# Kernel optimization log

Measured on AMD Instinct MI355X. Metric: run time of the kernel, lower is better.

Reference implementation:

```python
import jax, jax.numpy as jnp
import numpy as np

B = 65536
LAYERS = [256, 512, 512, 256]


def setup_inputs() -> dict:
    key = jax.random.key(0)
    ks = jax.random.split(key, 10)
    inp = {"data": jax.random.normal(ks[0], (B, LAYERS[0]), dtype=jnp.float32)}
    for i in range(3):
        n_in, n_out = LAYERS[i], LAYERS[i + 1]
        # link weights ~ U[0,1) like random.random(); bias params[0] zeroed in torch code
        inp[f"W{i+1}"] = jax.random.uniform(ks[1 + 3 * i], (n_in, n_out), dtype=jnp.float32)
        inp[f"b{i+1}"] = jnp.zeros((n_out,), dtype=jnp.float32)
        # per-node activation params a = params[1:6], torch.rand init
        inp[f"a{i+1}"] = jax.random.uniform(ks[2 + 3 * i], (n_out, 5), dtype=jnp.float32)
    return inp


def _act(x, a):
    # x: [B, n], a: [n, 5]; a0*tanh(x)*sin(a1*x+a2) + a3*x + a4  (per-node params broadcast over batch)
    return a[:, 0] * jnp.tanh(x) * jnp.sin(a[:, 1] * x + a[:, 2]) + a[:, 3] * x + a[:, 4]


def reference(data, W1, b1, a1, W2, b2, a2, W3, b3, a3):
    h = _act(data @ W1 + b1, a1)
    h = _act(h @ W2 + b2, a2)
    h = _act(h @ W3 + b3, a3)
    return jax.nn.softmax(h, axis=1)
```

## Files before the change

### kernel.cpp

```cpp
#include <hip/hip_runtime.h>

#define BATCH 65536

typedef float f32x4 __attribute__((ext_vector_type(4)));
typedef _Float16 f16x8 __attribute__((ext_vector_type(8)));

__device__ __forceinline__ void async_ld16(const void* g, void* l) {
  __builtin_amdgcn_global_load_lds(
      (const __attribute__((address_space(1))) void*)g,
      (__attribute__((address_space(3))) void*)l, 16, 0, 0);
}

__device__ __forceinline__ float act_f(float x, float a0, float a1, float a2,
                                       float a3, float a4) {
  float ax = fabsf(x);
  float e = __builtin_amdgcn_exp2f(ax * -2.8853900817779268f);
  float th = (1.0f - e) * __builtin_amdgcn_rcpf(1.0f + e);
  th = copysignf(th, x);
  float arg = fmaf(a1, x, a2);
  float rev = arg * 0.15915494309189535f;
  rev -= floorf(rev);
  float s = __builtin_amdgcn_sinf(rev);
  return fmaf(a3, x, fmaf(a0 * th, s, a4));
}

__global__ __launch_bounds__(256) void splitT_k(const float* __restrict__ W,
                                                _Float16* __restrict__ hi,
                                                _Float16* __restrict__ lo,
                                                int K, int N) {
  const int i = blockIdx.x * 256 + threadIdx.x;
  if (i >= K * N) return;
  const int n = i / K, k = i % K;
  const float w = W[(size_t)k * N + n];
  const _Float16 h = (_Float16)w;
  hi[i] = h;
  lo[i] = (_Float16)(w - (float)h);
}

__device__ __forceinline__ f32x4 mfma3(f16x8 ah, f16x8 al, f16x8 bh, f16x8 bl,
                                       f32x4 c) {
  c = __builtin_amdgcn_mfma_f32_16x16x32_f16(ah, bh, c, 0, 0, 0);
  c = __builtin_amdgcn_mfma_f32_16x16x32_f16(ah, bl, c, 0, 0, 0);
  c = __builtin_amdgcn_mfma_f32_16x16x32_f16(al, bh, c, 0, 0, 0);
  return c;
}

template <bool AF32, bool FINAL>
__global__ __launch_bounds__(256, 4) void gemm_act(
    const float* __restrict__ Af, const _Float16* __restrict__ Ahi,
    const _Float16* __restrict__ Alo, const _Float16* __restrict__ Bhi,
    const _Float16* __restrict__ Blo, const float* __restrict__ bias,
    const float* __restrict__ ap, _Float16* __restrict__ Chi,
    _Float16* __restrict__ Clo, float* __restrict__ Cout, int K, int N) {
  __shared__ __align__(16) _Float16 sA[4096];
  __shared__ __align__(16) _Float16 sB[16384];

  const int tid = threadIdx.x;
  const int wv = tid >> 6;
  const int lane = tid & 63;
  const int wm = wv >> 1, wn = wv & 1;
  const int m16 = lane & 15, quad = lane >> 4;
  const int col0 = blockIdx.x * 256;
  const int row0 = blockIdx.y * 64;

  f32x4 acc[2][8];
  const f32x4 zero = {0.f, 0.f, 0.f, 0.f};
#pragma unroll
  for (int i = 0; i < 2; ++i)
#pragma unroll
    for (int j = 0; j < 8; ++j) acc[i][j] = zero;

  const int nk = K >> 5;
  for (int kt = 0; kt < nk; ++kt) {
    const int k0 = kt << 5;
    if (AF32) {
      float* sAf = (float*)sA;
#pragma unroll
      for (int t = 0; t < 2; ++t) {
        const int c = wv * 2 + t;
        const int r = c * 8 + (lane >> 3);
        const size_t ga = (size_t)(row0 + r) * K + k0 + (lane & 7) * 4;
        async_ld16(Af + ga, (void*)&sAf[c * 256]);
      }
    } else {
      const int r = wv * 16 + (lane >> 2);
      const size_t ga = (size_t)(row0 + r) * K + k0 + (lane & 3) * 8;
      async_ld16(Ahi + ga, (void*)&sA[wv * 512]);
      async_ld16(Alo + ga, (void*)&sA[2048 + wv * 512]);
    }
#pragma unroll
    for (int t = 0; t < 4; ++t) {
      const int c = wv * 4 + t;
      const int col = c * 16 + (lane >> 2);
      const size_t gb = (size_t)(col0 + col) * K + k0 + (lane & 3) * 8;
      async_ld16(Bhi + gb, (void*)&sB[c * 512]);
      async_ld16(Blo + gb, (void*)&sB[8192 + c * 512]);
    }
    __syncthreads();

    f16x8 ah[2], al[2];
#pragma unroll
    for (int tm = 0; tm < 2; ++tm) {
      const int arow = wm * 32 + tm * 16 + m16;
      if (AF32) {
        const float* pa = (const float*)sA + arow * 32 + quad * 8;
        const f32x4 x0 = *(const f32x4*)pa;
        const f32x4 x1 = *(const f32x4*)(pa + 4);
#pragma unroll
        for (int j = 0; j < 4; ++j) {
          const _Float16 h0 = (_Float16)x0[j];
          ah[tm][j] = h0;
          al[tm][j] = (_Float16)(x0[j] - (float)h0);
          const _Float16 h1 = (_Float16)x1[j];
          ah[tm][4 + j] = h1;
          al[tm][4 + j] = (_Float16)(x1[j] - (float)h1);
        }
      } else {
        ah[tm] = *(const f16x8*)&sA[arow * 32 + quad * 8];
        al[tm] = *(const f16x8*)&sA[2048 + arow * 32 + quad * 8];
      }
    }
#pragma unroll
    for (int tn = 0; tn < 8; ++tn) {
      const int bcol = wn * 128 + tn * 16 + m16;
      const f16x8 bh = *(const f16x8*)&sB[bcol * 32 + quad * 8];
      const f16x8 bl = *(const f16x8*)&sB[8192 + bcol * 32 + quad * 8];
#pragma unroll
      for (int tm = 0; tm < 2; ++tm)
        acc[tm][tn] = mfma3(ah[tm], al[tm], bh, bl, acc[tm][tn]);
    }
    __syncthreads();
  }

  if (FINAL) {
    float* const redf = (float*)sA;
    float* const rowm = (float*)sA + 128;
    float* const rowi = (float*)sA + 192;
#pragma unroll
    for (int tn = 0; tn < 8; ++tn) {
      const int col = col0 + wn * 128 + tn * 16 + m16;
      const float bs = bias[col];
      const float p0 = ap[col * 5 + 0];
      const float p1 = ap[col * 5 + 1];
      const float p2 = ap[col * 5 + 2];
      const float p3 = ap[col * 5 + 3];
      const float p4 = ap[col * 5 + 4];
#pragma unroll
      for (int tm = 0; tm < 2; ++tm)
#pragma unroll
        for (int r = 0; r < 4; ++r)
          acc[tm][tn][r] = act_f(acc[tm][tn][r] + bs, p0, p1, p2, p3, p4);
    }
#pragma unroll
    for (int tm = 0; tm < 2; ++tm)
#pragma unroll
      for (int r = 0; r < 4; ++r) {
        float m = acc[tm][0][r];
#pragma unroll
        for (int tn = 1; tn < 8; ++tn) m = fmaxf(m, acc[tm][tn][r]);
#pragma unroll
        for (int off = 1; off < 16; off <<= 1) m = fmaxf(m, __shfl_xor(m, off));
        if (m16 == 0) {
          const int rowl = wm * 32 + tm * 16 + quad * 4 + r;
          redf[wn * 64 + rowl] = m;
        }
      }
    __syncthreads();
    if (tid < 64) rowm[tid] = fmaxf(redf[tid], redf[64 + tid]);
    __syncthreads();
#pragma unroll
    for (int tm = 0; tm < 2; ++tm)
#pragma unroll
      for (int r = 0; r < 4; ++r) {
        const int rowl = wm * 32 + tm * 16 + quad * 4 + r;
        const float m = rowm[rowl];
        float s = 0.f;
#pragma unroll
        for (int tn = 0; tn < 8; ++tn) {
          const float e = __builtin_amdgcn_exp2f((acc[tm][tn][r] - m) *
                                                 1.4426950408889634f);
          acc[tm][tn][r] = e;
          s += e;
        }
#pragma unroll
        for (int off = 1; off < 16; off <<= 1) s += __shfl_xor(s, off);
        if (m16 == 0) redf[wn * 64 + rowl] = s;
      }
    __syncthreads();
    if (tid < 64) rowi[tid] = __builtin_amdgcn_rcpf(redf[tid] + redf[64 + tid]);
    __syncthreads();
#pragma unroll
    for (int tm = 0; tm < 2; ++tm)
#pragma unroll
      for (int r = 0; r < 4; ++r) {
        const int rowl = wm * 32 + tm * 16 + quad * 4 + r;
        const float inv = rowi[rowl];
#pragma unroll
        for (int tn = 0; tn < 8; ++tn) {
          const int col = col0 + wn * 128 + tn * 16 + m16;
          Cout[(size_t)(row0 + rowl) * 256 + col] = acc[tm][tn][r] * inv;
        }
      }
  } else {
#pragma unroll
    for (int tn = 0; tn < 8; ++tn) {
      const int col = col0 + wn * 128 + tn * 16 + m16;
      const float bs = bias[col];
      const float p0 = ap[col * 5 + 0];
      const float p1 = ap[col * 5 + 1];
      const float p2 = ap[col * 5 + 2];
      const float p3 = ap[col * 5 + 3];
      const float p4 = ap[col * 5 + 4];
#pragma unroll
      for (int tm = 0; tm < 2; ++tm) {
        const int row = row0 + wm * 32 + tm * 16 + quad * 4;
#pragma unroll
        for (int r = 0; r < 4; ++r) {
          const float y = act_f(acc[tm][tn][r] + bs, p0, p1, p2, p3, p4);
          const size_t o = (size_t)(row + r) * N + col;
          const _Float16 h = (_Float16)y;
          Chi[o] = h;
          Clo[o] = (_Float16)(y - (float)h);
        }
      }
    }
  }
}

extern "C" void kernel_launch(void* const* d_in, const int* in_sizes, int n_in,
                              void* d_out, int out_size, void* d_ws,
                              size_t ws_size, hipStream_t stream) {
  const float* data = (const float*)d_in[0];
  const float* W1 = (const float*)d_in[1];
  const float* b1 = (const float*)d_in[2];
  const float* a1 = (const float*)d_in[3];
  const float* W2 = (const float*)d_in[4];
  const float* b2 = (const float*)d_in[5];
  const float* a2 = (const float*)d_in[6];
  const float* W3 = (const float*)d_in[7];
  const float* b3 = (const float*)d_in[8];
  const float* a3 = (const float*)d_in[9];
  float* out = (float*)d_out;

  char* ws = (char*)d_ws;
  const size_t KB = 1024, MB = 1024 * 1024;
  _Float16* w1hi = (_Float16*)(ws + 0 * KB);
  _Float16* w1lo = (_Float16*)(ws + 256 * KB);
  _Float16* w2hi = (_Float16*)(ws + 512 * KB);
  _Float16* w2lo = (_Float16*)(ws + 1024 * KB);
  _Float16* w3hi = (_Float16*)(ws + 1536 * KB);
  _Float16* w3lo = (_Float16*)(ws + 1792 * KB);
  _Float16* h1hi = (_Float16*)(ws + 2 * MB);
  _Float16* h1lo = (_Float16*)(ws + 2 * MB + (size_t)BATCH * 512 * 2);
  _Float16* h2lo = (_Float16*)(ws + 2 * MB + (size_t)BATCH * 512 * 4);
  _Float16* h2hi = (_Float16*)d_out;

  splitT_k<<<(256 * 512 + 255) / 256, 256, 0, stream>>>(W1, w1hi, w1lo, 256, 512);
  splitT_k<<<(512 * 512 + 255) / 256, 256, 0, stream>>>(W2, w2hi, w2lo, 512, 512);
  splitT_k<<<(512 * 256 + 255) / 256, 256, 0, stream>>>(W3, w3hi, w3lo, 512, 256);

  gemm_act<true, false><<<dim3(2, BATCH / 64), 256, 0, stream>>>(
      data, nullptr, nullptr, w1hi, w1lo, b1, a1, h1hi, h1lo, nullptr, 256, 512);
  gemm_act<false, false><<<dim3(2, BATCH / 64), 256, 0, stream>>>(
      nullptr, h1hi, h1lo, w2hi, w2lo, b2, a2, h2hi, h2lo, nullptr, 512, 512);
  gemm_act<false, true><<<dim3(1, BATCH / 64), 256, 0, stream>>>(
      nullptr, h2hi, h2lo, w3hi, w3lo, b3, a3, nullptr, nullptr, out, 512, 256);
}
```

Baseline: 427.2 us.

## Use square 128x128 tiles with XOR-swizzled LDS for hidden layers

Splits the templated kernel into a 128x128-tile kernel for the first two layers and a dedicated 64x256 kernel for the final layer with softmax. The square tiles are meant to balance A and B reuse and reduce global traffic per MFMA, and an XOR swizzle on the LDS chunk index is meant to remove bank conflicts on the fragment reads. The trade-offs are more accumulator registers per wave (16 tiles) and twice the A staging space at the same occupancy target.

```diff
diff --git a/kernel.cpp b/kernel.cpp
--- a/kernel.cpp
+++ b/kernel.cpp
@@ -45,30 +45,31 @@
   return c;
 }
 
-template <bool AF32, bool FINAL>
-__global__ __launch_bounds__(256, 4) void gemm_act(
+template <bool AF32>
+__global__ __launch_bounds__(256, 4) void gemm128(
     const float* __restrict__ Af, const _Float16* __restrict__ Ahi,
     const _Float16* __restrict__ Alo, const _Float16* __restrict__ Bhi,
     const _Float16* __restrict__ Blo, const float* __restrict__ bias,
     const float* __restrict__ ap, _Float16* __restrict__ Chi,
-    _Float16* __restrict__ Clo, float* __restrict__ Cout, int K, int N) {
-  __shared__ __align__(16) _Float16 sA[4096];
-  __shared__ __align__(16) _Float16 sB[16384];
+    _Float16* __restrict__ Clo, int K, int N) {
+  __shared__ __align__(16) _Float16 sA[8192];
+  __shared__ __align__(16) _Float16 sB[8192];
 
   const int tid = threadIdx.x;
   const int wv = tid >> 6;
   const int lane = tid & 63;
   const int wm = wv >> 1, wn = wv & 1;
   const int m16 = lane & 15, quad = lane >> 4;
-  const int col0 = blockIdx.x * 256;
-  const int row0 = blockIdx.y * 64;
-
-  f32x4 acc[2][8];
+  const int qsw = quad ^ (m16 & 3);
+  const int col0 = blockIdx.x * 128;
+  const int row0 = blockIdx.y * 128;
+
+  f32x4 acc[4][4];
   const f32x4 zero = {0.f, 0.f, 0.f, 0.f};
 #pragma unroll
-  for (int i = 0; i < 2; ++i)
-#pragma unroll
-    for (int j = 0; j < 8; ++j) acc[i][j] = zero;
+  for (int i = 0; i < 4; ++i)
+#pragma unroll
+    for (int j = 0; j < 4; ++j) acc[i][j] = zero;
 
   const int nk = K >> 5;
   for (int kt = 0; kt < nk; ++kt) {
@@ -76,36 +77,45 @@
     if (AF32) {
       float* sAf = (float*)sA;
 #pragma unroll
+      for (int t = 0; t < 4; ++t) {
+        const int c = wv * 4 + t;
+        const int r = c * 8 + (lane >> 3);
+        const int sl = (lane & 7) ^ (r & 7);
+        const size_t ga = (size_t)(row0 + r) * K + k0 + sl * 4;
+        async_ld16(Af + ga, (void*)&sAf[c * 256]);
+      }
+    } else {
+#pragma unroll
       for (int t = 0; t < 2; ++t) {
         const int c = wv * 2 + t;
-        const int r = c * 8 + (lane >> 3);
-        const size_t ga = (size_t)(row0 + r) * K + k0 + (lane & 7) * 4;
-        async_ld16(Af + ga, (void*)&sAf[c * 256]);
-      }
-    } else {
-      const int r = wv * 16 + (lane >> 2);
-      const size_t ga = (size_t)(row0 + r) * K + k0 + (lane & 3) * 8;
-      async_ld16(Ahi + ga, (void*)&sA[wv * 512]);
-      async_ld16(Alo + ga, (void*)&sA[2048 + wv * 512]);
-    }
-#pragma unroll
-    for (int t = 0; t < 4; ++t) {
-      const int c = wv * 4 + t;
+        const int r = c * 16 + (lane >> 2);
+        const int sl = (lane & 3) ^ (r & 3);
+        const size_t ga = (size_t)(row0 + r) * K + k0 + sl * 8;
+        async_ld16(Ahi + ga, (void*)&sA[c * 512]);
+        async_ld16(Alo + ga, (void*)&sA[4096 + c * 512]);
+      }
+    }
+#pragma unroll
+    for (int t = 0; t < 2; ++t) {
+      const int c = wv * 2 + t;
       const int col = c * 16 + (lane >> 2);
-      const size_t gb = (size_t)(col0 + col) * K + k0 + (lane & 3) * 8;
+      const int sl = (lane & 3) ^ (col & 3);
+      const size_t gb = (size_t)(col0 + col) * K + k0 + sl * 8;
       async_ld16(Bhi + gb, (void*)&sB[c * 512]);
-      async_ld16(Blo + gb, (void*)&sB[8192 + c * 512]);
+      async_ld16(Blo + gb, (void*)&sB[4096 + c * 512]);
     }
     __syncthreads();
 
-    f16x8 ah[2], al[2];
-#pragma unroll
-    for (int tm = 0; tm < 2; ++tm) {
-      const int arow = wm * 32 + tm * 16 + m16;
+    f16x8 ah[4], al[4];
+#pragma unroll
+    for (int tm = 0; tm < 4; ++tm) {
+      const int arow = wm * 64 + tm * 16 + m16;
       if (AF32) {
-        const float* pa = (const float*)sA + arow * 32 + quad * 8;
-        const f32x4 x0 = *(const f32x4*)pa;
-        const f32x4 x1 = *(const f32x4*)(pa + 4);
+        const float* pa = (const float*)sA + arow * 32;
+        const int s0 = (2 * quad) ^ (m16 & 7);
+        const int s1 = (2 * quad + 1) ^ (m16 & 7);
+        const f32x4 x0 = *(const f32x4*)(pa + s0 * 4);
+        const f32x4 x1 = *(const f32x4*)(pa + s1 * 4);
 #pragma unroll
         for (int j = 0; j < 4; ++j) {
           const _Float16 h0 = (_Float16)x0[j];
@@ -116,9 +126,93 @@
           al[tm][4 + j] = (_Float16)(x1[j] - (float)h1);
         }
       } else {
-        ah[tm] = *(const f16x8*)&sA[arow * 32 + quad * 8];
-        al[tm] = *(const f16x8*)&sA[2048 + arow * 32 + quad * 8];
-      }
+        ah[tm] = *(const f16x8*)&sA[arow * 32 + qsw * 8];
+        al[tm] = *(const f16x8*)&sA[4096 + arow * 32 + qsw * 8];
+      }
+    }
+#pragma unroll
+    for (int tn = 0; tn < 4; ++tn) {
+      const int bcol = wn * 64 + tn * 16 + m16;
+      const f16x8 bh = *(const f16x8*)&sB[bcol * 32 + qsw * 8];
+      const f16x8 bl = *(const f16x8*)&sB[4096 + bcol * 32 + qsw * 8];
+#pragma unroll
+      for (int tm = 0; tm < 4; ++tm)
+        acc[tm][tn] = mfma3(ah[tm], al[tm], bh, bl, acc[tm][tn]);
+    }
+    __syncthreads();
+  }
+
+#pragma unroll
+  for (int tn = 0; tn < 4; ++tn) {
+    const int col = col0 + wn * 64 + tn * 16 + m16;
+    const float bs = bias[col];
+    const float p0 = ap[col * 5 + 0];
+    const float p1 = ap[col * 5 + 1];
+    const float p2 = ap[col * 5 + 2];
+    const float p3 = ap[col * 5 + 3];
+    const float p4 = ap[col * 5 + 4];
+#pragma unroll
+    for (int tm = 0; tm < 4; ++tm) {
+      const int row = row0 + wm * 64 + tm * 16 + quad * 4;
+#pragma unroll
+      for (int r = 0; r < 4; ++r) {
+        const float y = act_f(acc[tm][tn][r] + bs, p0, p1, p2, p3, p4);
+        const size_t o = (size_t)(row + r) * N + col;
+        const _Float16 h = (_Float16)y;
+        Chi[o] = h;
+        Clo[o] = (_Float16)(y - (float)h);
+      }
+    }
+  }
+}
+
+__global__ __launch_bounds__(256, 4) void gemm_final(
+    const _Float16* __restrict__ Ahi, const _Float16* __restrict__ Alo,
+    const _Float16* __restrict__ Bhi, const _Float16* __restrict__ Blo,
+    const float* __restrict__ bias, const float* __restrict__ ap,
+    float* __restrict__ Cout, int K) {
+  __shared__ __align__(16) _Float16 sA[4096];
+  __shared__ __align__(16) _Float16 sB[16384];
+
+  const int tid = threadIdx.x;
+  const int wv = tid >> 6;
+  const int lane = tid & 63;
+  const int wm = wv >> 1, wn = wv & 1;
+  const int m16 = lane & 15, quad = lane >> 4;
+  const int row0 = blockIdx.x * 64;
+
+  f32x4 acc[2][8];
+  const f32x4 zero = {0.f, 0.f, 0.f, 0.f};
+#pragma unroll
+  for (int i = 0; i < 2; ++i)
+#pragma unroll
+    for (int j = 0; j < 8; ++j) acc[i][j] = zero;
+
+  const int nk = K >> 5;
+  for (int kt = 0; kt < nk; ++kt) {
+    const int k0 = kt << 5;
+    {
+      const int r = wv * 16 + (lane >> 2);
+      const size_t ga = (size_t)(row0 + r) * K + k0 + (lane & 3) * 8;
+      async_ld16(Ahi + ga, (void*)&sA[wv * 512]);
+      async_ld16(Alo + ga, (void*)&sA[2048 + wv * 512]);
+    }
+#pragma unroll
+    for (int t = 0; t < 4; ++t) {
+      const int c = wv * 4 + t;
+      const int col = c * 16 + (lane >> 2);
+      const size_t gb = (size_t)col * K + k0 + (lane & 3) * 8;
+      async_ld16(Bhi + gb, (void*)&sB[c * 512]);
+      async_ld16(Blo + gb, (void*)&sB[8192 + c * 512]);
+    }
+    __syncthreads();
+
+    f16x8 ah[2], al[2];
+#pragma unroll
+    for (int tm = 0; tm < 2; ++tm) {
+      const int arow = wm * 32 + tm * 16 + m16;
+      ah[tm] = *(const f16x8*)&sA[arow * 32 + quad * 8];
+      al[tm] = *(const f16x8*)&sA[2048 + arow * 32 + quad * 8];
     }
 #pragma unroll
     for (int tn = 0; tn < 8; ++tn) {
@@ -132,99 +226,74 @@
     __syncthreads();
   }
 
-  if (FINAL) {
-    float* const redf = (float*)sA;
-    float* const rowm = (float*)sA + 128;
-    float* const rowi = (float*)sA + 192;
-#pragma unroll
-    for (int tn = 0; tn < 8; ++tn) {
-      const int col = col0 + wn * 128 + tn * 16 + m16;
-      const float bs = bias[col];
-      const float p0 = ap[col * 5 + 0];
-      const float p1 = ap[col * 5 + 1];
-      const float p2 = ap[col * 5 + 2];
-      const float p3 = ap[col * 5 + 3];
-      const float p4 = ap[col * 5 + 4];
-#pragma unroll
-      for (int tm = 0; tm < 2; ++tm)
-#pragma unroll
-        for (int r = 0; r < 4; ++r)
-          acc[tm][tn][r] = act_f(acc[tm][tn][r] + bs, p0, p1, p2, p3, p4);
-    }
+  float* const redf = (float*)sA;
+  float* const rowm = (float*)sA + 128;
+  float* const rowi = (float*)sA + 192;
+#pragma unroll
+  for (int tn = 0; tn < 8; ++tn) {
+    const int col = wn * 128 + tn * 16 + m16;
+    const float bs = bias[col];
+    const float p0 = ap[col * 5 + 0];
+    const float p1 = ap[col * 5 + 1];
+    const float p2 = ap[col * 5 + 2];
+    const float p3 = ap[col * 5 + 3];
+    const float p4 = ap[col * 5 + 4];
 #pragma unroll
     for (int tm = 0; tm < 2; ++tm)
 #pragma unroll
-      for (int r = 0; r < 4; ++r) {
-        float m = acc[tm][0][r];
-#pragma unroll
-        for (int tn = 1; tn < 8; ++tn) m = fmaxf(m, acc[tm][tn][r]);
-#pragma unroll
-        for (int off = 1; off < 16; off <<= 1) m = fmaxf(m, __shfl_xor(m, off));
-        if (m16 == 0) {
-          const int rowl = wm * 32 + tm * 16 + quad * 4 + r;
-          redf[wn * 64 + rowl] = m;
-        }
-      }
-    __syncthreads();
-    if (tid < 64) rowm[tid] = fmaxf(redf[tid], redf[64 + tid]);
-    __syncthreads();
-#pragma unroll
-    for (int tm = 0; tm < 2; ++tm)
-#pragma unroll
-      for (int r = 0; r < 4; ++r) {
+      for (int r = 0; r < 4; ++r)
+        acc[tm][tn][r] = act_f(acc[tm][tn][r] + bs, p0, p1, p2, p3, p4);
+  }
+#pragma unroll
+  for (int tm = 0; tm < 2; ++tm)
+#pragma unroll
+    for (int r = 0; r < 4; ++r) {
+      float m = acc[tm][0][r];
+#pragma unroll
+      for (int tn = 1; tn < 8; ++tn) m = fmaxf(m, acc[tm][tn][r]);
+#pragma unroll
+      for (int off = 1; off < 16; off <<= 1) m = fmaxf(m, __shfl_xor(m, off));
+      if (m16 == 0) {
         const int rowl = wm * 32 + tm * 16 + quad * 4 + r;
-        const float m = rowm[rowl];
-        float s = 0.f;
-#pragma unroll
-        for (int tn = 0; tn < 8; ++tn) {
-          const float e = __builtin_amdgcn_exp2f((acc[tm][tn][r] - m) *
-                                                 1.4426950408889634f);
-          acc[tm][tn][r] = e;
-          s += e;
-        }
-#pragma unroll
-        for (int off = 1; off < 16; off <<= 1) s += __shfl_xor(s, off);
-        if (m16 == 0) redf[wn * 64 + rowl] = s;
-      }
-    __syncthreads();
-    if (tid < 64) rowi[tid] = __builtin_amdgcn_rcpf(redf[tid] + redf[64 + tid]);
-    __syncthreads();
-#pragma unroll
-    for (int tm = 0; tm < 2; ++tm)
-#pragma unroll
-      for (int r = 0; r < 4; ++r) {
-        const int rowl = wm * 32 + tm * 16 + quad * 4 + r;
-        const float inv = rowi[rowl];
-#pragma unroll
-        for (int tn = 0; tn < 8; ++tn) {
-          const int col = col0 + wn * 128 + tn * 16 + m16;
-          Cout[(size_t)(row0 + rowl) * 256 + col] = acc[tm][tn][r] * inv;
-        }
-      }
-  } else {
-#pragma unroll
-    for (int tn = 0; tn < 8; ++tn) {
-      const int col = col0 + wn * 128 + tn * 16 + m16;
-      const float bs = bias[col];
-      const float p0 = ap[col * 5 + 0];
-      const float p1 = ap[col * 5 + 1];
-      const float p2 = ap[col * 5 + 2];
-      const float p3 = ap[col * 5 + 3];
-      const float p4 = ap[col * 5 + 4];
-#pragma unroll
-      for (int tm = 0; tm < 2; ++tm) {
-        const int row = row0 + wm * 32 + tm * 16 + quad * 4;
-#pragma unroll
-        for (int r = 0; r < 4; ++r) {
-          const float y = act_f(acc[tm][tn][r] + bs, p0, p1, p2, p3, p4);
-          const size_t o = (size_t)(row + r) * N + col;
-          const _Float16 h = (_Float16)y;
-          Chi[o] = h;
-          Clo[o] = (_Float16)(y - (float)h);
-        }
-      }
-    }
-  }
+        redf[wn * 64 + rowl] = m;
+      }
+    }
+  __syncthreads();
+  if (tid < 64) rowm[tid] = fmaxf(redf[tid], redf[64 + tid]);
+  __syncthreads();
+#pragma unroll
+  for (int tm = 0; tm < 2; ++tm)
+#pragma unroll
+    for (int r = 0; r < 4; ++r) {
+      const int rowl = wm * 32 + tm * 16 + quad * 4 + r;
+      const float m = rowm[rowl];
+      float s = 0.f;
+#pragma unroll
+      for (int tn = 0; tn < 8; ++tn) {
+        const float e =
+            __builtin_amdgcn_exp2f((acc[tm][tn][r] - m) * 1.4426950408889634f);
+        acc[tm][tn][r] = e;
+        s += e;
+      }
+#pragma unroll
+      for (int off = 1; off < 16; off <<= 1) s += __shfl_xor(s, off);
+      if (m16 == 0) redf[wn * 64 + rowl] = s;
+    }
+  __syncthreads();
+  if (tid < 64) rowi[tid] = __builtin_amdgcn_rcpf(redf[tid] + redf[64 + tid]);
+  __syncthreads();
+#pragma unroll
+  for (int tm = 0; tm < 2; ++tm)
+#pragma unroll
+    for (int r = 0; r < 4; ++r) {
+      const int rowl = wm * 32 + tm * 16 + quad * 4 + r;
+      const float inv = rowi[rowl];
+#pragma unroll
+      for (int tn = 0; tn < 8; ++tn) {
+        const int col = wn * 128 + tn * 16 + m16;
+        Cout[(size_t)(row0 + rowl) * 256 + col] = acc[tm][tn][r] * inv;
+      }
+    }
 }
 
 extern "C" void kernel_launch(void* const* d_in, const int* in_sizes, int n_in,
@@ -259,10 +328,10 @@
   splitT_k<<<(512 * 512 + 255) / 256, 256, 0, stream>>>(W2, w2hi, w2lo, 512, 512);
   splitT_k<<<(512 * 256 + 255) / 256, 256, 0, stream>>>(W3, w3hi, w3lo, 512, 256);
 
-  gemm_act<true, false><<<dim3(2, BATCH / 64), 256, 0, stream>>>(
-      data, nullptr, nullptr, w1hi, w1lo, b1, a1, h1hi, h1lo, nullptr, 256, 512);
-  gemm_act<false, false><<<dim3(2, BATCH / 64), 256, 0, stream>>>(
-      nullptr, h1hi, h1lo, w2hi, w2lo, b2, a2, h2hi, h2lo, nullptr, 512, 512);
-  gemm_act<false, true><<<dim3(1, BATCH / 64), 256, 0, stream>>>(
-      nullptr, h2hi, h2lo, w3hi, w3lo, b3, a3, nullptr, nullptr, out, 512, 256);
-}
+  gemm128<true><<<dim3(4, BATCH / 128), 256, 0, stream>>>(
+      data, nullptr, nullptr, w1hi, w1lo, b1, a1, h1hi, h1lo, 256, 512);
+  gemm128<false><<<dim3(4, BATCH / 128), 256, 0, stream>>>(
+      nullptr, h1hi, h1lo, w2hi, w2lo, b2, a2, h2hi, h2lo, 512, 512);
+  gemm_final<<<BATCH / 64, 256, 0, stream>>>(h2hi, h2lo, w3hi, w3lo, b3, a3,
+                                             out, 512);
+}
```

Measured after the change: 496.5 us. +16.2%, slower.

## Enlarge GEMM block tile to 128x256 with 8 waves and XOR-swizzle LDS

Applied to the files above, without the earlier changes.

Doubles the block tile to 128 rows by 256 columns using 512 threads (2x4 waves, each computing a 64x64 sub-tile), so weight tiles are reused across twice as many rows. It also XOR-swizzles the 16-byte chunk positions in LDS for both A and B, on the async store side and the read side, to reduce bank conflicts on the MFMA operand loads. The softmax reduction is widened to combine four column-wave partials. The cost is more LDS per block and launch bounds of 512x4, which may push register pressure and lower occupancy.

```diff
diff --git a/kernel.cpp b/kernel.cpp
--- a/kernel.cpp
+++ b/kernel.cpp
@@ -46,29 +46,30 @@
 }
 
 template <bool AF32, bool FINAL>
-__global__ __launch_bounds__(256, 4) void gemm_act(
+__global__ __launch_bounds__(512, 4) void gemm_act(
     const float* __restrict__ Af, const _Float16* __restrict__ Ahi,
     const _Float16* __restrict__ Alo, const _Float16* __restrict__ Bhi,
     const _Float16* __restrict__ Blo, const float* __restrict__ bias,
     const float* __restrict__ ap, _Float16* __restrict__ Chi,
     _Float16* __restrict__ Clo, float* __restrict__ Cout, int K, int N) {
-  __shared__ __align__(16) _Float16 sA[4096];
+  __shared__ __align__(16) _Float16 sA[8192];
   __shared__ __align__(16) _Float16 sB[16384];
 
   const int tid = threadIdx.x;
   const int wv = tid >> 6;
   const int lane = tid & 63;
-  const int wm = wv >> 1, wn = wv & 1;
+  const int wm = wv >> 2, wn = wv & 3;
   const int m16 = lane & 15, quad = lane >> 4;
+  const int qsw = quad ^ (m16 & 3);
   const int col0 = blockIdx.x * 256;
-  const int row0 = blockIdx.y * 64;
-
-  f32x4 acc[2][8];
+  const int row0 = blockIdx.y * 128;
+
+  f32x4 acc[4][4];
   const f32x4 zero = {0.f, 0.f, 0.f, 0.f};
 #pragma unroll
-  for (int i = 0; i < 2; ++i)
-#pragma unroll
-    for (int j = 0; j < 8; ++j) acc[i][j] = zero;
+  for (int i = 0; i < 4; ++i)
+#pragma unroll
+    for (int j = 0; j < 4; ++j) acc[i][j] = zero;
 
   const int nk = K >> 5;
   for (int kt = 0; kt < nk; ++kt) {
@@ -79,33 +80,38 @@
       for (int t = 0; t < 2; ++t) {
         const int c = wv * 2 + t;
         const int r = c * 8 + (lane >> 3);
-        const size_t ga = (size_t)(row0 + r) * K + k0 + (lane & 7) * 4;
+        const int sl = (lane & 7) ^ (r & 7);
+        const size_t ga = (size_t)(row0 + r) * K + k0 + sl * 4;
         async_ld16(Af + ga, (void*)&sAf[c * 256]);
       }
     } else {
       const int r = wv * 16 + (lane >> 2);
-      const size_t ga = (size_t)(row0 + r) * K + k0 + (lane & 3) * 8;
+      const int sl = (lane & 3) ^ (r & 3);
+      const size_t ga = (size_t)(row0 + r) * K + k0 + sl * 8;
       async_ld16(Ahi + ga, (void*)&sA[wv * 512]);
-      async_ld16(Alo + ga, (void*)&sA[2048 + wv * 512]);
-    }
-#pragma unroll
-    for (int t = 0; t < 4; ++t) {
-      const int c = wv * 4 + t;
+      async_ld16(Alo + ga, (void*)&sA[4096 + wv * 512]);
+    }
+#pragma unroll
+    for (int t = 0; t < 2; ++t) {
+      const int c = wv * 2 + t;
       const int col = c * 16 + (lane >> 2);
-      const size_t gb = (size_t)(col0 + col) * K + k0 + (lane & 3) * 8;
+      const int sl = (lane & 3) ^ (col & 3);
+      const size_t gb = (size_t)(col0 + col) * K + k0 + sl * 8;
       async_ld16(Bhi + gb, (void*)&sB[c * 512]);
       async_ld16(Blo + gb, (void*)&sB[8192 + c * 512]);
     }
     __syncthreads();
 
-    f16x8 ah[2], al[2];
-#pragma unroll
-    for (int tm = 0; tm < 2; ++tm) {
-      const int arow = wm * 32 + tm * 16 + m16;
+    f16x8 ah[4], al[4];
+#pragma unroll
+    for (int tm = 0; tm < 4; ++tm) {
+      const int arow = wm * 64 + tm * 16 + m16;
       if (AF32) {
-        const float* pa = (const float*)sA + arow * 32 + quad * 8;
-        const f32x4 x0 = *(const f32x4*)pa;
-        const f32x4 x1 = *(const f32x4*)(pa + 4);
+        const float* pa = (const float*)sA + arow * 32;
+        const int s0 = (2 * quad) ^ (m16 & 7);
+        const int s1 = (2 * quad + 1) ^ (m16 & 7);
+        const f32x4 x0 = *(const f32x4*)(pa + s0 * 4);
+        const f32x4 x1 = *(const f32x4*)(pa + s1 * 4);
 #pragma unroll
         for (int j = 0; j < 4; ++j) {
           const _Float16 h0 = (_Float16)x0[j];
@@ -116,17 +122,17 @@
           al[tm][4 + j] = (_Float16)(x1[j] - (float)h1);
         }
       } else {
-        ah[tm] = *(const f16x8*)&sA[arow * 32 + quad * 8];
-        al[tm] = *(const f16x8*)&sA[2048 + arow * 32 + quad * 8];
-      }
-    }
-#pragma unroll
-    for (int tn = 0; tn < 8; ++tn) {
-      const int bcol = wn * 128 + tn * 16 + m16;
-      const f16x8 bh = *(const f16x8*)&sB[bcol * 32 + quad * 8];
-      const f16x8 bl = *(const f16x8*)&sB[8192 + bcol * 32 + quad * 8];
-#pragma unroll
-      for (int tm = 0; tm < 2; ++tm)
+        ah[tm] = *(const f16x8*)&sA[arow * 32 + qsw * 8];
+        al[tm] = *(const f16x8*)&sA[4096 + arow * 32 + qsw * 8];
+      }
+    }
+#pragma unroll
+    for (int tn = 0; tn < 4; ++tn) {
+      const int bcol = wn * 64 + tn * 16 + m16;
+      const f16x8 bh = *(const f16x8*)&sB[bcol * 32 + qsw * 8];
+      const f16x8 bl = *(const f16x8*)&sB[8192 + bcol * 32 + qsw * 8];
+#pragma unroll
+      for (int tm = 0; tm < 4; ++tm)
         acc[tm][tn] = mfma3(ah[tm], al[tm], bh, bl, acc[tm][tn]);
     }
     __syncthreads();
@@ -134,11 +140,11 @@
 
   if (FINAL) {
     float* const redf = (float*)sA;
-    float* const rowm = (float*)sA + 128;
-    float* const rowi = (float*)sA + 192;
-#pragma unroll
-    for (int tn = 0; tn < 8; ++tn) {
-      const int col = col0 + wn * 128 + tn * 16 + m16;
+    float* const rowm = (float*)sA + 512;
+    float* const rowi = (float*)sA + 640;
+#pragma unroll
+    for (int tn = 0; tn < 4; ++tn) {
+      const int col = wn * 64 + tn * 16 + m16;
       const float bs = bias[col];
       const float p0 = ap[col * 5 + 0];
       const float p1 = ap[col * 5 + 1];
@@ -146,37 +152,38 @@
       const float p3 = ap[col * 5 + 3];
       const float p4 = ap[col * 5 + 4];
 #pragma unroll
-      for (int tm = 0; tm < 2; ++tm)
+      for (int tm = 0; tm < 4; ++tm)
 #pragma unroll
         for (int r = 0; r < 4; ++r)
           acc[tm][tn][r] = act_f(acc[tm][tn][r] + bs, p0, p1, p2, p3, p4);
     }
 #pragma unroll
-    for (int tm = 0; tm < 2; ++tm)
+    for (int tm = 0; tm < 4; ++tm)
 #pragma unroll
       for (int r = 0; r < 4; ++r) {
-        float m = acc[tm][0][r];
-#pragma unroll
-        for (int tn = 1; tn < 8; ++tn) m = fmaxf(m, acc[tm][tn][r]);
+        float m = fmaxf(fmaxf(acc[tm][0][r], acc[tm][1][r]),
+                        fmaxf(acc[tm][2][r], acc[tm][3][r]));
 #pragma unroll
         for (int off = 1; off < 16; off <<= 1) m = fmaxf(m, __shfl_xor(m, off));
         if (m16 == 0) {
-          const int rowl = wm * 32 + tm * 16 + quad * 4 + r;
-          redf[wn * 64 + rowl] = m;
-        }
-      }
-    __syncthreads();
-    if (tid < 64) rowm[tid] = fmaxf(redf[tid], redf[64 + tid]);
-    __syncthreads();
-#pragma unroll
-    for (int tm = 0; tm < 2; ++tm)
+          const int rowl = wm * 64 + tm * 16 + quad * 4 + r;
+          redf[wn * 128 + rowl] = m;
+        }
+      }
+    __syncthreads();
+    if (tid < 128)
+      rowm[tid] = fmaxf(fmaxf(redf[tid], redf[128 + tid]),
+                        fmaxf(redf[256 + tid], redf[384 + tid]));
+    __syncthreads();
+#pragma unroll
+    for (int tm = 0; tm < 4; ++tm)
 #pragma unroll
       for (int r = 0; r < 4; ++r) {
-        const int rowl = wm * 32 + tm * 16 + quad * 4 + r;
+        const int rowl = wm * 64 + tm * 16 + quad * 4 + r;
         const float m = rowm[rowl];
         float s = 0.f;
 #pragma unroll
-        for (int tn = 0; tn < 8; ++tn) {
+        for (int tn = 0; tn < 4; ++tn) {
           const float e = __builtin_amdgcn_exp2f((acc[tm][tn][r] - m) *
                                                  1.4426950408889634f);
           acc[tm][tn][r] = e;
@@ -184,27 +191,29 @@
         }
 #pragma unroll
         for (int off = 1; off < 16; off <<= 1) s += __shfl_xor(s, off);
-        if (m16 == 0) redf[wn * 64 + rowl] = s;
-      }
-    __syncthreads();
-    if (tid < 64) rowi[tid] = __builtin_amdgcn_rcpf(redf[tid] + redf[64 + tid]);
-    __syncthreads();
-#pragma unroll
-    for (int tm = 0; tm < 2; ++tm)
+        if (m16 == 0) redf[wn * 128 + rowl] = s;
+      }
+    __syncthreads();
+    if (tid < 128)
+      rowi[tid] = __builtin_amdgcn_rcpf(redf[tid] + redf[128 + tid] +
+                                        redf[256 + tid] + redf[384 + tid]);
+    __syncthreads();
+#pragma unroll
+    for (int tm = 0; tm < 4; ++tm)
 #pragma unroll
       for (int r = 0; r < 4; ++r) {
-        const int rowl = wm * 32 + tm * 16 + quad * 4 + r;
+        const int rowl = wm * 64 + tm * 16 + quad * 4 + r;
         const float inv = rowi[rowl];
 #pragma unroll
-        for (int tn = 0; tn < 8; ++tn) {
-          const int col = col0 + wn * 128 + tn * 16 + m16;
+        for (int tn = 0; tn < 4; ++tn) {
+          const int col = wn * 64 + tn * 16 + m16;
           Cout[(size_t)(row0 + rowl) * 256 + col] = acc[tm][tn][r] * inv;
         }
       }
   } else {
 #pragma unroll
-    for (int tn = 0; tn < 8; ++tn) {
-      const int col = col0 + wn * 128 + tn * 16 + m16;
+    for (int tn = 0; tn < 4; ++tn) {
+      const int col = col0 + wn * 64 + tn * 16 + m16;
       const float bs = bias[col];
       const float p0 = ap[col * 5 + 0];
       const float p1 = ap[col * 5 + 1];
@@ -212,8 +221,8 @@
       const float p3 = ap[col * 5 + 3];
       const float p4 = ap[col * 5 + 4];
 #pragma unroll
-      for (int tm = 0; tm < 2; ++tm) {
-        const int row = row0 + wm * 32 + tm * 16 + quad * 4;
+      for (int tm = 0; tm < 4; ++tm) {
+        const int row = row0 + wm * 64 + tm * 16 + quad * 4;
 #pragma unroll
         for (int r = 0; r < 4; ++r) {
           const float y = act_f(acc[tm][tn][r] + bs, p0, p1, p2, p3, p4);
@@ -259,10 +268,10 @@
   splitT_k<<<(512 * 512 + 255) / 256, 256, 0, stream>>>(W2, w2hi, w2lo, 512, 512);
   splitT_k<<<(512 * 256 + 255) / 256, 256, 0, stream>>>(W3, w3hi, w3lo, 512, 256);
 
-  gemm_act<true, false><<<dim3(2, BATCH / 64), 256, 0, stream>>>(
+  gemm_act<true, false><<<dim3(2, BATCH / 128), 512, 0, stream>>>(
       data, nullptr, nullptr, w1hi, w1lo, b1, a1, h1hi, h1lo, nullptr, 256, 512);
-  gemm_act<false, false><<<dim3(2, BATCH / 64), 256, 0, stream>>>(
+  gemm_act<false, false><<<dim3(2, BATCH / 128), 512, 0, stream>>>(
       nullptr, h1hi, h1lo, w2hi, w2lo, b2, a2, h2hi, h2lo, nullptr, 512, 512);
-  gemm_act<false, true><<<dim3(1, BATCH / 64), 256, 0, stream>>>(
+  gemm_act<false, true><<<dim3(1, BATCH / 128), 512, 0, stream>>>(
       nullptr, h2hi, h2lo, w3hi, w3lo, b3, a3, nullptr, nullptr, out, 512, 256);
 }
```

New measurement: 527.9 us. 23.6% more time.
